# Kernel optimization log

Measured on AMD Instinct MI355X. Metric: run time of the kernel, lower is better.

Reference implementation:

```python
import jax, jax.numpy as jnp
import numpy as np

BATCH, SEQ, D_MODEL = 4, 4096, 1024
HEADS, DIM_HEAD = 8, 128
BUCKET, N_HASHES = 64, 4
N_BUCKETS = SEQ // BUCKET
LN_EPS = 1e-3
SELF_ATTN_VAL = -5e4   # TOKEN_SELF_ATTN_VALUE in reformer_pytorch
MASK_VAL = -1e9        # stand-in for max_neg_value on padded keys
UNIT_EPS = 1e-6        # make_unit_length epsilon


def setup_inputs() -> dict:
    key = jax.random.key(0)
    ks = jax.random.split(key, 8)
    s = 0.02
    return {
        "i": jax.random.normal(ks[0], (BATCH, SEQ, D_MODEL), jnp.float32),
        "mask": jnp.ones((BATCH, SEQ), dtype=bool),
        "rotations": jax.random.normal(ks[1], (DIM_HEAD, N_HASHES, N_BUCKETS // 2), jnp.float32),
        "Wqk": jax.random.normal(ks[2], (D_MODEL, D_MODEL), jnp.float32) * s,
        "Wv": jax.random.normal(ks[3], (D_MODEL, D_MODEL), jnp.float32) * s,
        "Wo": jax.random.normal(ks[4], (D_MODEL, D_MODEL), jnp.float32) * s,
        "bo": jnp.zeros((D_MODEL,), jnp.float32),
        "ln_g": jnp.ones((D_MODEL,), jnp.float32),
        "ln_b": jnp.zeros((D_MODEL,), jnp.float32),
    }


def _look_one_back(x):
    # concat each chunk with the previous chunk along the within-chunk axis
    return jnp.concatenate([x, jnp.roll(x, 1, axis=1)], axis=2)


def _lsh_attention(qk, v, mask, rotations):
    # qk, v: (B, T, d) with B = batch*heads; mask: (B, T) bool
    B, T, d = qk.shape
    # --- hash into buckets (no grad through hashing) ---
    rot = jnp.einsum('btd,dhr->bhtr', jax.lax.stop_gradient(qk), rotations)
    rot = jnp.concatenate([rot, -rot], axis=-1)              # (B, nh, T, n_buckets)
    buckets = jnp.argmax(rot, axis=-1)                       # (B, nh, T)
    offsets = (jnp.arange(N_HASHES) * N_BUCKETS)[None, :, None]
    buckets = (buckets + offsets).reshape(B, N_HASHES * T)
    # --- stable bucket sort of tokens ---
    ticker = jnp.arange(N_HASHES * T)
    buckets_and_t = buckets * T + (ticker % T)               # unique keys
    sticker = jnp.argsort(buckets_and_t, axis=-1)            # (B, nh*T)
    undo_sort = jnp.argsort(sticker, axis=-1)
    st = sticker % T                                         # original positions
    sqk = jnp.take_along_axis(qk, st[..., None], axis=1)
    sv = jnp.take_along_axis(v, st[..., None], axis=1)
    # --- chunked local attention ---
    n_chunks = N_HASHES * N_BUCKETS
    bq_t = st.reshape(B, n_chunks, BUCKET)
    bq = sqk.reshape(B, n_chunks, BUCKET, d)
    nrm = jnp.linalg.norm(bq, axis=-1, keepdims=True)
    bk = bq / jnp.maximum(nrm, UNIT_EPS)                     # shared-QK: keys are unit-length queries
    bv = sv.reshape(B, n_chunks, BUCKET, d)
    bk = _look_one_back(bk)                                  # (B, C, 2*BUCKET, d)
    bv = _look_one_back(bv)
    bkv_t = _look_one_back(bq_t)                             # (B, C, 2*BUCKET)
    dots = jnp.einsum('bcid,bcjd->bcij', bq, bk) * (d ** -0.5)
    # input (padding) mask
    mq = jnp.take_along_axis(mask, st, axis=1).reshape(B, n_chunks, BUCKET)
    mkv = _look_one_back(mq)
    dots = jnp.where(mq[..., :, None] & mkv[..., None, :], dots, MASK_VAL)
    # avoid attending to self except as a fallback
    dots = jnp.where(bq_t[..., :, None] == bkv_t[..., None, :], SELF_ATTN_VAL, dots)
    dots_lse = jax.nn.logsumexp(dots, axis=-1, keepdims=True)  # (B, C, BUCKET, 1)
    probs = jnp.exp(dots - dots_lse)
    bo = jnp.einsum('bcij,bcjd->bcid', probs, bv)
    so = bo.reshape(B, N_HASHES * T, d)
    slogits = dots_lse.reshape(B, N_HASHES * T)
    # --- unsort and combine hash rounds via softmax over per-round logsumexps ---
    o = jnp.take_along_axis(so, undo_sort[..., None], axis=1).reshape(B, N_HASHES, T, d)
    logits = jnp.take_along_axis(slogits, undo_sort, axis=1).reshape(B, N_HASHES, T, 1)
    w = jnp.exp(logits - jax.nn.logsumexp(logits, axis=1, keepdims=True))
    return jnp.sum(o * w, axis=1)                            # (B, T, d)


def _forward(i, mask, rotations, Wqk, Wv, Wo, bo, ln_g, ln_b):
    b, t, dm = i.shape
    qk = i @ Wqk
    v = i @ Wv

    def split_heads(x):
        return x.reshape(b, t, HEADS, DIM_HEAD).transpose(0, 2, 1, 3).reshape(b * HEADS, t, DIM_HEAD)

    qk, v = split_heads(qk), split_heads(v)
    m = jnp.repeat(mask, HEADS, axis=0)                      # (b*h, t)
    out = _lsh_attention(qk, v, m, rotations)
    out = out.reshape(b, HEADS, t, DIM_HEAD).transpose(0, 2, 1, 3).reshape(b, t, dm)
    out = out @ Wo + bo                                      # to_out
    # eval-mode dropout is identity; then LayerNorm(eps=1e-3)
    mu = out.mean(-1, keepdims=True)
    var = out.var(-1, keepdims=True)
    return (out - mu) / jnp.sqrt(var + LN_EPS) * ln_g + ln_b


def reference(i, mask, rotations, Wqk, Wv, Wo, bo, ln_g, ln_b):
    return _forward(i, mask, rotations, Wqk, Wv, Wo, bo, ln_g, ln_b)
```

## Files before the change

### kernel.cpp

```cpp
#include <hip/hip_runtime.h>
#include <hip/hip_bf16.h>

#define B_   4
#define T_   4096
#define DM   1024
#define H_   8
#define DH   128
#define BHN  32
#define NH   4
#define NB   64
#define NT   16384
#define NC   256
#define SCALE_ 0.08838834764831845f
#define SELF_VAL -50000.0f
#define FLAG_CAP 262144
#define GAP_THR 2.5e-3f

typedef unsigned short u16;
typedef __attribute__((ext_vector_type(8))) short short8;
typedef __attribute__((ext_vector_type(8))) unsigned short us8;
typedef __attribute__((ext_vector_type(4))) float f32x4;

__device__ __forceinline__ float bf2f(u16 x) {
  union { unsigned u; float f; } c; c.u = ((unsigned)x) << 16; return c.f;
}
__device__ __forceinline__ u16 f2bf(float f) {
  union { float f; unsigned u; } c; c.f = f;
  unsigned r = (c.u + 0x7FFFu + ((c.u >> 16) & 1u)) >> 16;
  return (u16)r;
}

__global__ __launch_bounds__(256) void k_isplit(
    const float* __restrict__ I, u16* __restrict__ ih, u16* __restrict__ il) {
  size_t idx = ((size_t)blockIdx.x * 256 + threadIdx.x) * 8;
  us8 vh, vl;
  #pragma unroll
  for (int e = 0; e < 8; ++e) {
    float x = I[idx + e];
    u16 h = f2bf(x);
    vh[e] = h;
    vl[e] = f2bf(x - bf2f(h));
  }
  *(us8*)(ih + idx) = vh;
  *(us8*)(il + idx) = vl;
}

__global__ __launch_bounds__(256) void k_wr(
    const float* __restrict__ Wqk, const float* __restrict__ R, double* __restrict__ WR) {
  __shared__ float lR[128][128];
  int tid = threadIdx.x;
  int k0 = blockIdx.x * 64, h = blockIdx.y;
  #pragma unroll
  for (int q = 0; q < 64; ++q)
    ((float*)lR)[q * 256 + tid] = R[q * 256 + tid];
  __syncthreads();
  int k = k0 + (tid >> 2);
  int hr0 = (tid & 3) * 32;
  double acc[32];
  #pragma unroll
  for (int j = 0; j < 32; ++j) acc[j] = 0.0;
  for (int d = 0; d < 128; ++d) {
    double w = (double)Wqk[(size_t)k * DM + h * DH + d];
    #pragma unroll
    for (int j = 0; j < 32; ++j)
      acc[j] = fma(w, (double)lR[d][hr0 + j], acc[j]);
  }
  double* o = WR + ((size_t)h * 1024 + k) * 128 + hr0;
  #pragma unroll
  for (int j = 0; j < 32; ++j) o[j] = acc[j];
}

__global__ __launch_bounds__(256) void k_wsplit(
    const float* __restrict__ Wqk, const float* __restrict__ Wv,
    const float* __restrict__ Wo, const double* __restrict__ WR,
    u16* __restrict__ Wqkt, u16* __restrict__ Wvt, u16* __restrict__ Wot,
    u16* __restrict__ WR2t) {
  int tid = blockIdx.x * 256 + threadIdx.x;
  int k = tid >> 7, n8 = (tid & 127) << 3;
  #pragma unroll
  for (int j = 0; j < 8; ++j) {
    int n = n8 + j;
    Wqkt[(size_t)n * 1024 + k] = f2bf(Wqk[(size_t)k * 1024 + n]);
    Wvt [(size_t)n * 1024 + k] = f2bf(Wv [(size_t)k * 1024 + n]);
    Wot [(size_t)n * 1024 + k] = f2bf(Wo [(size_t)k * 1024 + n]);
    double w = WR[((size_t)(n >> 7) * 1024 + k) * 128 + (n & 127)];
    u16 wh = f2bf((float)w);
    u16 wl = f2bf((float)(w - (double)bf2f(wh)));
    WR2t[(size_t)n * 2048 + k] = wh;
    WR2t[(size_t)n * 2048 + 1024 + k] = wl;
  }
}

__global__ void k_zero(unsigned* flagc) { if (threadIdx.x == 0) *flagc = 0; }

template <int EPI>
__global__ __launch_bounds__(256) void k_gemm(
    const u16* __restrict__ A, const u16* __restrict__ A2,
    const u16* __restrict__ Bt, int K,
    u16* __restrict__ outb, float* __restrict__ outf, const float* __restrict__ bias,
    int* __restrict__ buckets, unsigned* __restrict__ flagc, int* __restrict__ flags) {
  __shared__ u16 smbuf[2][128][72];
  int tid = threadIdx.x;
  int m0 = blockIdx.x * 128, n0 = blockIdx.y * 128;
  int w = tid >> 6, lane = tid & 63;
  int wr = w >> 1, wc = w & 1;
  int arow = lane & 15, kg = lane >> 4;
  int srow = tid >> 1, shalf = tid & 1;
  const int ldb = (EPI == 2) ? 2048 : 1024;
  const u16* gA  = A  + (size_t)(m0 + srow) * 1024 + shalf * 32;
  const u16* gA2 = (EPI == 2) ? (A2 + (size_t)(m0 + srow) * 1024 + shalf * 32) : nullptr;
  const u16* gB  = Bt + (size_t)(n0 + srow) * ldb + shalf * 32;

  auto load_ab = [&](int k0v, us8* ra_, us8* rb_) {
    const u16 *pa_, *pb_;
    if constexpr (EPI == 2) {
      pa_ = ((k0v < 2048) ? gA : gA2) + (k0v & 1023);
      pb_ = gB + ((k0v < 2048) ? k0v : (k0v & 1023));
    } else {
      pa_ = gA + k0v;
      pb_ = gB + k0v;
    }
    #pragma unroll
    for (int q = 0; q < 4; ++q) {
      ra_[q] = *(const us8*)(pa_ + q * 8);
      rb_[q] = *(const us8*)(pb_ + q * 8);
    }
  };

  f32x4 acc[4][4];
  #pragma unroll
  for (int m = 0; m < 4; ++m)
    #pragma unroll
    for (int n = 0; n < 4; ++n) acc[m][n] = (f32x4){0.f, 0.f, 0.f, 0.f};

  us8 ra[4], rb[4];
  load_ab(0, ra, rb);

  for (int k0 = 0; k0 < K; k0 += 64) {
    __syncthreads();
    #pragma unroll
    for (int q = 0; q < 4; ++q) {
      *(us8*)(&smbuf[0][srow][shalf * 32 + q * 8]) = ra[q];
      *(us8*)(&smbuf[1][srow][shalf * 32 + q * 8]) = rb[q];
    }
    __syncthreads();
    if (k0 + 64 < K) load_ab(k0 + 64, ra, rb);
    #pragma unroll
    for (int ks = 0; ks < 2; ++ks) {
      short8 af[4], bf[4];
      #pragma unroll
      for (int m = 0; m < 4; ++m)
        af[m] = *(const short8*)(&smbuf[0][wr * 64 + m * 16 + arow][ks * 32 + kg * 8]);
      #pragma unroll
      for (int n = 0; n < 4; ++n)
        bf[n] = *(const short8*)(&smbuf[1][wc * 64 + n * 16 + arow][ks * 32 + kg * 8]);
      #pragma unroll
      for (int m = 0; m < 4; ++m)
        #pragma unroll
        for (int n = 0; n < 4; ++n)
          acc[m][n] = __builtin_amdgcn_mfma_f32_16x16x32_bf16(af[m], bf[n], acc[m][n], 0, 0, 0);
    }
  }

  if constexpr (EPI == 0) {
    #pragma unroll
    for (int m = 0; m < 4; ++m)
      #pragma unroll
      for (int n = 0; n < 4; ++n)
        #pragma unroll
        for (int r = 0; r < 4; ++r) {
          int orow = wr * 64 + m * 16 + kg * 4 + r;
          int ocol = wc * 64 + n * 16 + arow;
          outb[(size_t)(m0 + orow) * 1024 + n0 + ocol] = f2bf(acc[m][n][r]);
        }
  } else if constexpr (EPI == 1) {
    #pragma unroll
    for (int m = 0; m < 4; ++m)
      #pragma unroll
      for (int n = 0; n < 4; ++n)
        #pragma unroll
        for (int r = 0; r < 4; ++r) {
          int orow = wr * 64 + m * 16 + kg * 4 + r;
          int ocol = wc * 64 + n * 16 + arow;
          outf[(size_t)(m0 + orow) * 1024 + n0 + ocol] = acc[m][n][r] + bias[n0 + ocol];
        }
  } else {
    float (*sC)[132] = (float (*)[132])(&smbuf[0][0][0]);
    #pragma unroll
    for (int pass = 0; pass < 2; ++pass) {
      __syncthreads();
      if (wr == pass) {
        #pragma unroll
        for (int m = 0; m < 4; ++m)
          #pragma unroll
          for (int n = 0; n < 4; ++n)
            #pragma unroll
            for (int r = 0; r < 4; ++r)
              sC[m * 16 + kg * 4 + r][wc * 64 + n * 16 + arow] = acc[m][n][r];
      }
      __syncthreads();
      int tok = tid >> 2, hash = tid & 3;
      const float* rw = &sC[tok][hash * 32];
      float m1 = -3.4e38f, m2 = -3.4e38f; int bi = 0;
      #pragma unroll
      for (int j = 0; j < 32; ++j) {
        float vv = rw[j];
        if (vv > m1) { m2 = m1; m1 = vv; bi = j; }
        else if (vv > m2) m2 = vv;
      }
      #pragma unroll
      for (int j = 0; j < 32; ++j) {
        float vv = -rw[j];
        if (vv > m1) { m2 = m1; m1 = vv; bi = 32 + j; }
        else if (vv > m2) m2 = vv;
      }
      int bt = m0 + pass * 64 + tok;
      int b = bt >> 12, t = bt & 4095;
      buckets[((size_t)(b * 8 + blockIdx.y) * 4 + hash) * T_ + t] = bi;
      if (m1 - m2 < GAP_THR) {
        unsigned pos = atomicAdd(flagc, 1u);
        if (pos < FLAG_CAP) flags[pos] = (bt << 5) | ((int)blockIdx.y << 2) | hash;
      }
    }
  }
}

__global__ __launch_bounds__(64) void k_fb(
    const float* __restrict__ I, const double* __restrict__ WR,
    const unsigned* __restrict__ flagc, const int* __restrict__ flags,
    int* __restrict__ buckets) {
  unsigned n = *flagc; if (n > FLAG_CAP) n = FLAG_CAP;
  int lane = threadIdx.x;
  for (unsigned it = blockIdx.x; it < n; it += gridDim.x) {
    int f = flags[it];
    int bt = f >> 5, h = (f >> 2) & 7, hash = f & 3;
    int j = lane & 31, half = lane >> 5;
    const float* ip = I + (size_t)bt * 1024 + half * 512;
    const double* wp = WR + ((size_t)h * 1024 + half * 512) * 128 + hash * 32 + j;
    double acc = 0.0;
    for (int k = 0; k < 512; ++k)
      acc = fma((double)ip[k], wp[(size_t)k * 128], acc);
    acc += __shfl_down(acc, 32, 64);
    double bv = acc; int bi = j;
    double vneg = -acc;
    if (vneg > bv) { bv = vneg; bi = 32 + j; }
    #pragma unroll
    for (int m = 1; m < 32; m <<= 1) {
      double ov = __shfl_xor(bv, m, 64);
      int oi = __shfl_xor(bi, m, 64);
      if (ov > bv || (ov == bv && oi < bi)) { bv = ov; bi = oi; }
    }
    if (lane == 0) {
      int b = bt >> 12, t = bt & 4095;
      buckets[((size_t)(b * 8 + h) * 4 + hash) * T_ + t] = bi;
    }
  }
}

__global__ __launch_bounds__(64) void k_sort(
    const int* __restrict__ buckets, int* __restrict__ st, int* __restrict__ inv) {
  __shared__ int hist[64][65];
  __shared__ int base[64];
  int bh = blockIdx.x, r = blockIdx.y;
  int m = threadIdx.x;
  #pragma unroll
  for (int b = 0; b < 64; ++b) hist[b][m] = 0;
  __syncthreads();
  const int* bk = buckets + ((size_t)bh * NH + r) * T_;
  for (int q = 0; q < 64; ++q) hist[bk[m * 64 + q]][m]++;
  __syncthreads();
  {
    int run = 0;
    for (int c = 0; c < 64; ++c) { int x = hist[m][c]; hist[m][c] = run; run += x; }
    base[m] = run;
  }
  __syncthreads();
  if (m == 0) {
    int s = 0;
    for (int b = 0; b < 64; ++b) { int x = base[b]; base[b] = s; s += x; }
  }
  __syncthreads();
  int* stb = st + (size_t)bh * NT + (size_t)r * T_;
  int* ivb = inv + (size_t)bh * NT + (size_t)r * T_;
  for (int q = 0; q < 64; ++q) {
    int t = m * 64 + q;
    int b = bk[t];
    int pos = base[b] + hist[b][m]++;
    stb[pos] = t;
    ivb[t] = r * T_ + pos;
  }
}

__global__ __launch_bounds__(256) void k_attn(
    const u16* __restrict__ qk, const u16* __restrict__ V, const int* __restrict__ st,
    u16* __restrict__ o_s, float* __restrict__ slog) {
  __shared__ u16 kbuf[128][136];
  __shared__ u16 pbuf[64][136];
  __shared__ int tks[128];
  float* psum   = (float*)&pbuf[0][0];
  float* recipn = (float*)&pbuf[4][0];
  int tid = threadIdx.x;
  int bh = blockIdx.x, chunk = blockIdx.y;
  int bb_ = bh >> 3, hh_ = bh & 7;
  const int* stb = st + (size_t)bh * NT;
  if (tid < 128) {
    int j = tid;
    int p = (j < 64) ? (chunk * 64 + j)
                     : (((chunk + NC - 1) % NC) * 64 + (j - 64));
    tks[j] = stb[p];
  }
  __syncthreads();
  {
    int j = tid & 127, half = tid >> 7;
    const ushort4* rp = (const ushort4*)(qk + ((size_t)(bb_ * T_ + tks[j])) * DM + hh_ * DH + half * 64);
    ushort4* dp = (ushort4*)(&kbuf[j][half * 64]);
    float ss = 0.f;
    #pragma unroll
    for (int c = 0; c < 16; ++c) {
      ushort4 x = rp[c];
      float f0 = bf2f(x.x), f1 = bf2f(x.y), f2 = bf2f(x.z), f3 = bf2f(x.w);
      ss += f0 * f0 + f1 * f1 + f2 * f2 + f3 * f3;
      dp[c] = x;
    }
    psum[j * 2 + half] = ss;
  }
  __syncthreads();
  if (tid < 128) {
    float n = sqrtf(psum[tid * 2] + psum[tid * 2 + 1]);
    recipn[tid] = 1.f / fmaxf(n, 1e-6f);
  }
  __syncthreads();

  int w = tid >> 6, lane = tid & 63;
  int arow = lane & 15, kgrp = lane >> 4;

  f32x4 acc[8];
  #pragma unroll
  for (int n = 0; n < 8; ++n) acc[n] = (f32x4){0.f, 0.f, 0.f, 0.f};
  #pragma unroll
  for (int kk = 0; kk < 4; ++kk) {
    short8 a = *(const short8*)(&kbuf[w * 16 + arow][kk * 32 + kgrp * 8]);
    #pragma unroll
    for (int n = 0; n < 8; ++n) {
      short8 bb = *(const short8*)(&kbuf[n * 16 + arow][kk * 32 + kgrp * 8]);
      acc[n] = __builtin_amdgcn_mfma_f32_16x16x32_bf16(a, bb, acc[n], 0, 0, 0);
    }
  }

  int ti[4];
  #pragma unroll
  for (int r = 0; r < 4; ++r) ti[r] = tks[w * 16 + kgrp * 4 + r];
  float vals[8][4];
  float rmax[4] = {-3.0e38f, -3.0e38f, -3.0e38f, -3.0e38f};
  #pragma unroll
  for (int n = 0; n < 8; ++n) {
    int j = n * 16 + arow;
    float rc = recipn[j] * SCALE_;
    int tj = tks[j];
    #pragma unroll
    for (int r = 0; r < 4; ++r) {
      float d = acc[n][r] * rc;
      if (ti[r] == tj) d = SELF_VAL;
      vals[n][r] = d;
      rmax[r] = fmaxf(rmax[r], d);
    }
  }
  __syncthreads();
  #pragma unroll
  for (int m = 1; m <= 8; m <<= 1) {
    #pragma unroll
    for (int r = 0; r < 4; ++r) rmax[r] = fmaxf(rmax[r], __shfl_xor(rmax[r], m, 64));
  }
  float rsum[4] = {0.f, 0.f, 0.f, 0.f};
  #pragma unroll
  for (int n = 0; n < 8; ++n) {
    #pragma unroll
    for (int r = 0; r < 4; ++r) {
      float e = __expf(vals[n][r] - rmax[r]);
      vals[n][r] = e;
      rsum[r] += e;
    }
  }
  #pragma unroll
  for (int m = 1; m <= 8; m <<= 1) {
    #pragma unroll
    for (int r = 0; r < 4; ++r) rsum[r] += __shfl_xor(rsum[r], m, 64);
  }
  float rinv[4], lse[4];
  #pragma unroll
  for (int r = 0; r < 4; ++r) {
    rinv[r] = 1.f / rsum[r];
    lse[r] = rmax[r] + __logf(rsum[r]);
  }
  if (arow == 0) {
    #pragma unroll
    for (int r = 0; r < 4; ++r)
      slog[(size_t)bh * NT + chunk * 64 + w * 16 + kgrp * 4 + r] = lse[r];
  }
  #pragma unroll
  for (int n = 0; n < 8; ++n) {
    #pragma unroll
    for (int r = 0; r < 4; ++r)
      pbuf[w * 16 + kgrp * 4 + r][n * 16 + arow] = f2bf(vals[n][r] * rinv[r]);
  }
  __syncthreads();
  {
    int j = tid & 127, half = tid >> 7;
    const ushort4* rp = (const ushort4*)(V + ((size_t)(bb_ * T_ + tks[j])) * DM + hh_ * DH + half * 64);
    #pragma unroll
    for (int c = 0; c < 16; ++c) {
      ushort4 x = rp[c];
      int d = half * 64 + c * 4;
      kbuf[d + 0][j] = x.x;
      kbuf[d + 1][j] = x.y;
      kbuf[d + 2][j] = x.z;
      kbuf[d + 3][j] = x.w;
    }
  }
  __syncthreads();

  f32x4 acc2[8];
  #pragma unroll
  for (int n = 0; n < 8; ++n) acc2[n] = (f32x4){0.f, 0.f, 0.f, 0.f};
  #pragma unroll
  for (int kk = 0; kk < 4; ++kk) {
    short8 a = *(const short8*)(&pbuf[w * 16 + arow][kk * 32 + kgrp * 8]);
    #pragma unroll
    for (int n = 0; n < 8; ++n) {
      short8 bb = *(const short8*)(&kbuf[n * 16 + arow][kk * 32 + kgrp * 8]);
      acc2[n] = __builtin_amdgcn_mfma_f32_16x16x32_bf16(a, bb, acc2[n], 0, 0, 0);
    }
  }
  u16* ob = o_s + ((size_t)bh * NT + (size_t)chunk * 64) * DH;
  #pragma unroll
  for (int n = 0; n < 8; ++n) {
    #pragma unroll
    for (int r = 0; r < 4; ++r)
      ob[(size_t)(w * 16 + kgrp * 4 + r) * DH + n * 16 + arow] = f2bf(acc2[n][r]);
  }
}

__global__ __launch_bounds__(256) void k_comb(
    const u16* __restrict__ o_s, const float* __restrict__ slog,
    const int* __restrict__ inv, u16* __restrict__ attn) {
  int tid = threadIdx.x;
  int bh = blockIdx.y;
  int t = blockIdx.x * 2 + (tid >> 7);
  int dd = tid & 127;
  const int* ivb = inv + (size_t)bh * NT;
  int p[4]; float l[4];
  #pragma unroll
  for (int r = 0; r < 4; ++r) {
    p[r] = ivb[r * T_ + t];
    l[r] = slog[(size_t)bh * NT + p[r]];
  }
  float m = fmaxf(fmaxf(l[0], l[1]), fmaxf(l[2], l[3]));
  float wv[4]; float wsum = 0.f;
  #pragma unroll
  for (int r = 0; r < 4; ++r) { wv[r] = __expf(l[r] - m); wsum += wv[r]; }
  float rs = 1.f / wsum;
  float o = 0.f;
  #pragma unroll
  for (int r = 0; r < 4; ++r)
    o += wv[r] * bf2f(o_s[((size_t)bh * NT + p[r]) * DH + dd]);
  o *= rs;
  int b = bh >> 3, h = bh & 7;
  attn[((size_t)(b * T_ + t)) * DM + h * DH + dd] = f2bf(o);
}

__global__ __launch_bounds__(256) void k_ln(
    const float* __restrict__ X, const float* __restrict__ G,
    const float* __restrict__ Bt, float* __restrict__ out) {
  __shared__ float w1[4], w2[4];
  int row = blockIdx.x, tid = threadIdx.x;
  const float4 v = ((const float4*)(X + (size_t)row * DM))[tid];
  float s = v.x + v.y + v.z + v.w;
  float s2 = v.x * v.x + v.y * v.y + v.z * v.z + v.w * v.w;
  #pragma unroll
  for (int m = 1; m < 64; m <<= 1) {
    s += __shfl_xor(s, m, 64);
    s2 += __shfl_xor(s2, m, 64);
  }
  int wid = tid >> 6;
  if ((tid & 63) == 0) { w1[wid] = s; w2[wid] = s2; }
  __syncthreads();
  float S = w1[0] + w1[1] + w1[2] + w1[3];
  float S2 = w2[0] + w2[1] + w2[2] + w2[3];
  float mu = S * (1.f / DM);
  float var = S2 * (1.f / DM) - mu * mu;
  float inv = 1.0f / sqrtf(var + 1e-3f);
  float4 g = ((const float4*)G)[tid];
  float4 b = ((const float4*)Bt)[tid];
  float4 o;
  o.x = (v.x - mu) * inv * g.x + b.x;
  o.y = (v.y - mu) * inv * g.y + b.y;
  o.z = (v.z - mu) * inv * g.z + b.z;
  o.w = (v.w - mu) * inv * g.w + b.w;
  ((float4*)(out + (size_t)row * DM))[tid] = o;
}

extern "C" void kernel_launch(void* const* d_in, const int* in_sizes, int n_in,
                              void* d_out, int out_size, void* d_ws, size_t ws_size,
                              hipStream_t stream) {
  const float* I   = (const float*)d_in[0];
  const float* R   = (const float*)d_in[2];
  const float* Wqk = (const float*)d_in[3];
  const float* Wv  = (const float*)d_in[4];
  const float* Wo  = (const float*)d_in[5];
  const float* bo  = (const float*)d_in[6];
  const float* lng = (const float*)d_in[7];
  const float* lnb = (const float*)d_in[8];

  char* ws = (char*)d_ws;
  const size_t MB = 1ull << 20;
  u16*      qk      = (u16*)(ws + 0);
  u16*      v       = (u16*)(ws + 32 * MB);
  u16*      o_s     = (u16*)(ws + 64 * MB);
  u16*      i_hi    = (u16*)(ws + 64 * MB);
  u16*      i_lo    = (u16*)(ws + 96 * MB);
  double*   WR      = (double*)(ws + 128 * MB);
  int*      flags   = (int*)(ws + 136 * MB);
  unsigned* flagc   = (unsigned*)(ws + 137 * MB);
  int*      buckets = (int*)(ws + 138 * MB);
  u16*      Wqkt    = (u16*)(ws + 140 * MB);
  u16*      Wvt     = (u16*)(ws + 142 * MB);
  u16*      WR2t    = (u16*)(ws + 144 * MB);
  float*    outp    = (float*)(ws + 64 * MB);
  int*      st      = (int*)(ws + 192 * MB);
  int*      inv     = (int*)(ws + 194 * MB);
  float*    slog    = (float*)(ws + 196 * MB);
  u16*      Wot     = (u16*)(ws + 198 * MB);
  u16*      attnb   = qk;
  float*    out     = (float*)d_out;

  k_isplit<<<8192, 256, 0, stream>>>(I, i_hi, i_lo);
  k_wr<<<dim3(16, 8), 256, 0, stream>>>(Wqk, R, WR);
  k_wsplit<<<512, 256, 0, stream>>>(Wqk, Wv, Wo, WR, Wqkt, Wvt, Wot, WR2t);
  k_zero<<<1, 64, 0, stream>>>(flagc);
  k_gemm<0><<<dim3(128, 8), 256, 0, stream>>>(i_hi, nullptr, Wqkt, 1024, qk, nullptr, nullptr, nullptr, nullptr, nullptr);
  k_gemm<0><<<dim3(128, 8), 256, 0, stream>>>(i_hi, nullptr, Wvt, 1024, v, nullptr, nullptr, nullptr, nullptr, nullptr);
  k_gemm<2><<<dim3(128, 8), 256, 0, stream>>>(i_hi, i_lo, WR2t, 3072, nullptr, nullptr, nullptr, buckets, flagc, flags);
  k_fb<<<1024, 64, 0, stream>>>(I, WR, flagc, flags, buckets);
  k_sort<<<dim3(BHN, NH), 64, 0, stream>>>(buckets, st, inv);
  k_attn<<<dim3(BHN, NC), 256, 0, stream>>>(qk, v, st, o_s, slog);
  k_comb<<<dim3(T_ / 2, BHN), 256, 0, stream>>>(o_s, slog, inv, attnb);
  k_gemm<1><<<dim3(128, 8), 256, 0, stream>>>(attnb, nullptr, Wot, 1024, nullptr, outp, bo, nullptr, nullptr, nullptr);
  k_ln<<<B_ * T_, 256, 0, stream>>>(outp, lng, lnb, out);
}
```

Measured before the change: 557.3 us.

## Fuse bucket hashing into qk GEMM epilogue via split-bf16 rotation MFMA

Replaces the separate qk GEMM and the WR-based hashing GEMM with one split-precision (hi/lo bf16, K=3072) qk GEMM. Its epilogue writes bf16 qk and then multiplies the fp32 qk tile by split-bf16 rotations with MFMA to produce bucket argmax and ambiguity flags. This removes one full 16384x1024x1024 GEMM pass and the WR2t preprocessing. In exchange the qk GEMM does three times the K work, and the hashing precision now depends on the split of the qk accumulator. It also swaps grid dimensions so the N tiles iterate fastest.

After: 673.2 us. 20.8% more time.

```diff
diff --git a/kernel.cpp b/kernel.cpp
--- a/kernel.cpp
+++ b/kernel.cpp
@@ -72,22 +72,32 @@
 
 __global__ __launch_bounds__(256) void k_wsplit(
     const float* __restrict__ Wqk, const float* __restrict__ Wv,
-    const float* __restrict__ Wo, const double* __restrict__ WR,
-    u16* __restrict__ Wqkt, u16* __restrict__ Wvt, u16* __restrict__ Wot,
-    u16* __restrict__ WR2t) {
+    const float* __restrict__ Wo,
+    u16* __restrict__ Wqk2t, u16* __restrict__ Wvt, u16* __restrict__ Wot) {
   int tid = blockIdx.x * 256 + threadIdx.x;
   int k = tid >> 7, n8 = (tid & 127) << 3;
   #pragma unroll
   for (int j = 0; j < 8; ++j) {
     int n = n8 + j;
-    Wqkt[(size_t)n * 1024 + k] = f2bf(Wqk[(size_t)k * 1024 + n]);
+    float wq = Wqk[(size_t)k * 1024 + n];
+    u16 qh = f2bf(wq);
+    Wqk2t[(size_t)n * 2048 + k] = qh;
+    Wqk2t[(size_t)n * 2048 + 1024 + k] = f2bf(wq - bf2f(qh));
     Wvt [(size_t)n * 1024 + k] = f2bf(Wv [(size_t)k * 1024 + n]);
     Wot [(size_t)n * 1024 + k] = f2bf(Wo [(size_t)k * 1024 + n]);
-    double w = WR[((size_t)(n >> 7) * 1024 + k) * 128 + (n & 127)];
-    u16 wh = f2bf((float)w);
-    u16 wl = f2bf((float)(w - (double)bf2f(wh)));
-    WR2t[(size_t)n * 2048 + k] = wh;
-    WR2t[(size_t)n * 2048 + 1024 + k] = wl;
+  }
+}
+
+__global__ __launch_bounds__(256) void k_rsplit(
+    const float* __restrict__ R, u16* __restrict__ R2m) {
+  int idx = blockIdx.x * 256 + threadIdx.x;
+  int hr = idx >> 4, d0 = (idx & 15) << 3;
+  #pragma unroll
+  for (int e = 0; e < 8; ++e) {
+    float x = R[(size_t)(d0 + e) * 128 + hr];
+    u16 h = f2bf(x);
+    R2m[(size_t)hr * 256 + d0 + e] = h;
+    R2m[(size_t)hr * 256 + 128 + d0 + e] = f2bf(x - bf2f(h));
   }
 }
 
@@ -98,22 +108,23 @@
     const u16* __restrict__ A, const u16* __restrict__ A2,
     const u16* __restrict__ Bt, int K,
     u16* __restrict__ outb, float* __restrict__ outf, const float* __restrict__ bias,
+    const u16* __restrict__ R2m,
     int* __restrict__ buckets, unsigned* __restrict__ flagc, int* __restrict__ flags) {
   __shared__ u16 smbuf[2][128][72];
   int tid = threadIdx.x;
-  int m0 = blockIdx.x * 128, n0 = blockIdx.y * 128;
+  int n0 = blockIdx.x * 128, m0 = blockIdx.y * 128;
   int w = tid >> 6, lane = tid & 63;
   int wr = w >> 1, wc = w & 1;
   int arow = lane & 15, kg = lane >> 4;
   int srow = tid >> 1, shalf = tid & 1;
-  const int ldb = (EPI == 2) ? 2048 : 1024;
+  const int ldb = (EPI == 3) ? 2048 : 1024;
   const u16* gA  = A  + (size_t)(m0 + srow) * 1024 + shalf * 32;
-  const u16* gA2 = (EPI == 2) ? (A2 + (size_t)(m0 + srow) * 1024 + shalf * 32) : nullptr;
+  const u16* gA2 = (EPI == 3) ? (A2 + (size_t)(m0 + srow) * 1024 + shalf * 32) : nullptr;
   const u16* gB  = Bt + (size_t)(n0 + srow) * ldb + shalf * 32;
 
   auto load_ab = [&](int k0v, us8* ra_, us8* rb_) {
     const u16 *pa_, *pb_;
-    if constexpr (EPI == 2) {
+    if constexpr (EPI == 3) {
       pa_ = ((k0v < 2048) ? gA : gA2) + (k0v & 1023);
       pb_ = gB + ((k0v < 2048) ? k0v : (k0v & 1023));
     } else {
@@ -185,19 +196,57 @@
           outf[(size_t)(m0 + orow) * 1024 + n0 + ocol] = acc[m][n][r] + bias[n0 + ocol];
         }
   } else {
-    float (*sC)[132] = (float (*)[132])(&smbuf[0][0][0]);
-    #pragma unroll
-    for (int pass = 0; pass < 2; ++pass) {
+    #pragma unroll
+    for (int m = 0; m < 4; ++m)
+      #pragma unroll
+      for (int n = 0; n < 4; ++n)
+        #pragma unroll
+        for (int r = 0; r < 4; ++r) {
+          int orow = wr * 64 + m * 16 + kg * 4 + r;
+          int ocol = wc * 64 + n * 16 + arow;
+          outb[(size_t)(m0 + orow) * 1024 + n0 + ocol] = f2bf(acc[m][n][r]);
+        }
+    u16   (*smA)[264] = (u16 (*)[264])(&smbuf[0][0][0]);
+    float (*sC)[132]  = (float (*)[132])(&smbuf[0][0][0]);
+    #pragma unroll
+    for (int h0 = 0; h0 < 2; ++h0) {
       __syncthreads();
-      if (wr == pass) {
+      if (wr == h0) {
         #pragma unroll
         for (int m = 0; m < 4; ++m)
           #pragma unroll
           for (int n = 0; n < 4; ++n)
             #pragma unroll
-            for (int r = 0; r < 4; ++r)
-              sC[m * 16 + kg * 4 + r][wc * 64 + n * 16 + arow] = acc[m][n][r];
+            for (int r = 0; r < 4; ++r) {
+              int row = m * 16 + kg * 4 + r;
+              int col = wc * 64 + n * 16 + arow;
+              float x = acc[m][n][r];
+              u16 hh = f2bf(x);
+              smA[row][col] = hh;
+              smA[row][128 + col] = f2bf(x - bf2f(hh));
+            }
       }
+      __syncthreads();
+      f32x4 accr[8];
+      #pragma unroll
+      for (int n = 0; n < 8; ++n) accr[n] = (f32x4){0.f, 0.f, 0.f, 0.f};
+      #pragma unroll
+      for (int ks = 0; ks < 12; ++ks) {
+        int ak = (ks < 8) ? ((ks & 3) * 32) : (128 + (ks - 8) * 32);
+        int bk = (ks < 4) ? (ks * 32) : ((ks < 8) ? (128 + (ks - 4) * 32) : ((ks - 8) * 32));
+        short8 a = *(const short8*)(&smA[w * 16 + arow][ak + kg * 8]);
+        #pragma unroll
+        for (int n = 0; n < 8; ++n) {
+          short8 bb = *(const short8*)(R2m + (size_t)(n * 16 + arow) * 256 + bk + kg * 8);
+          accr[n] = __builtin_amdgcn_mfma_f32_16x16x32_bf16(a, bb, accr[n], 0, 0, 0);
+        }
+      }
+      __syncthreads();
+      #pragma unroll
+      for (int n = 0; n < 8; ++n)
+        #pragma unroll
+        for (int r = 0; r < 4; ++r)
+          sC[w * 16 + kg * 4 + r][n * 16 + arow] = accr[n][r];
       __syncthreads();
       int tok = tid >> 2, hash = tid & 3;
       const float* rw = &sC[tok][hash * 32];
@@ -214,12 +263,12 @@
         if (vv > m1) { m2 = m1; m1 = vv; bi = 32 + j; }
         else if (vv > m2) m2 = vv;
       }
-      int bt = m0 + pass * 64 + tok;
+      int bt = m0 + h0 * 64 + tok;
       int b = bt >> 12, t = bt & 4095;
-      buckets[((size_t)(b * 8 + blockIdx.y) * 4 + hash) * T_ + t] = bi;
+      buckets[((size_t)(b * 8 + blockIdx.x) * 4 + hash) * T_ + t] = bi;
       if (m1 - m2 < GAP_THR) {
         unsigned pos = atomicAdd(flagc, 1u);
-        if (pos < FLAG_CAP) flags[pos] = (bt << 5) | ((int)blockIdx.y << 2) | hash;
+        if (pos < FLAG_CAP) flags[pos] = (bt << 5) | ((int)blockIdx.x << 2) | hash;
       }
     }
   }
@@ -522,9 +571,9 @@
   int*      flags   = (int*)(ws + 136 * MB);
   unsigned* flagc   = (unsigned*)(ws + 137 * MB);
   int*      buckets = (int*)(ws + 138 * MB);
-  u16*      Wqkt    = (u16*)(ws + 140 * MB);
-  u16*      Wvt     = (u16*)(ws + 142 * MB);
-  u16*      WR2t    = (u16*)(ws + 144 * MB);
+  u16*      Wvt     = (u16*)(ws + 140 * MB);
+  u16*      R2m     = (u16*)(ws + 142 * MB);
+  u16*      Wqk2t   = (u16*)(ws + 144 * MB);
   float*    outp    = (float*)(ws + 64 * MB);
   int*      st      = (int*)(ws + 192 * MB);
   int*      inv     = (int*)(ws + 194 * MB);
@@ -535,15 +584,15 @@
 
   k_isplit<<<8192, 256, 0, stream>>>(I, i_hi, i_lo);
   k_wr<<<dim3(16, 8), 256, 0, stream>>>(Wqk, R, WR);
-  k_wsplit<<<512, 256, 0, stream>>>(Wqk, Wv, Wo, WR, Wqkt, Wvt, Wot, WR2t);
+  k_wsplit<<<512, 256, 0, stream>>>(Wqk, Wv, Wo, Wqk2t, Wvt, Wot);
+  k_rsplit<<<8, 256, 0, stream>>>(R, R2m);
   k_zero<<<1, 64, 0, stream>>>(flagc);
-  k_gemm<0><<<dim3(128, 8), 256, 0, stream>>>(i_hi, nullptr, Wqkt, 1024, qk, nullptr, nullptr, nullptr, nullptr, nullptr);
-  k_gemm<0><<<dim3(128, 8), 256, 0, stream>>>(i_hi, nullptr, Wvt, 1024, v, nullptr, nullptr, nullptr, nullptr, nullptr);
-  k_gemm<2><<<dim3(128, 8), 256, 0, stream>>>(i_hi, i_lo, WR2t, 3072, nullptr, nullptr, nullptr, buckets, flagc, flags);
+  k_gemm<3><<<dim3(8, 128), 256, 0, stream>>>(i_hi, i_lo, Wqk2t, 3072, qk, nullptr, nullptr, R2m, buckets, flagc, flags);
+  k_gemm<0><<<dim3(8, 128), 256, 0, stream>>>(i_hi, nullptr, Wvt, 1024, v, nullptr, nullptr, nullptr, nullptr, nullptr, nullptr);
   k_fb<<<1024, 64, 0, stream>>>(I, WR, flagc, flags, buckets);
   k_sort<<<dim3(BHN, NH), 64, 0, stream>>>(buckets, st, inv);
   k_attn<<<dim3(BHN, NC), 256, 0, stream>>>(qk, v, st, o_s, slog);
   k_comb<<<dim3(T_ / 2, BHN), 256, 0, stream>>>(o_s, slog, inv, attnb);
-  k_gemm<1><<<dim3(128, 8), 256, 0, stream>>>(attnb, nullptr, Wot, 1024, nullptr, outp, bo, nullptr, nullptr, nullptr);
+  k_gemm<1><<<dim3(8, 128), 256, 0, stream>>>(attnb, nullptr, Wot, 1024, nullptr, outp, bo, nullptr, nullptr, nullptr, nullptr);
   k_ln<<<B_ * T_, 256, 0, stream>>>(outp, lng, lnb, out);
 }
```
